# Kernel optimization log

Measured on AMD Instinct MI355X. Metric: run time of the kernel, lower is better.

## Reference

```python
import jax, jax.numpy as jnp
import numpy as np

D_MODEL = 768
D_INNER = 1536      # d_model * expand
D_STATE = 128
D_CONV = 4
HEADDIM = 64
NHEADS = 24         # d_inner / headdim
CONV_DIM = D_INNER + 2 * D_STATE          # 1792
D_IN_PROJ = 2 * D_INNER + 2 * D_STATE + NHEADS  # 3352
EPS = 1e-5
BATCH, SEQLEN = 4, 2048


def setup_inputs() -> dict:
    key = jax.random.key(0)
    ks = jax.random.split(key, 8)
    u = jax.random.normal(ks[0], (BATCH, SEQLEN, D_MODEL), dtype=jnp.float32)
    W_in = jax.random.normal(ks[1], (D_IN_PROJ, D_MODEL), dtype=jnp.float32) * 0.02
    conv_w = jax.random.normal(ks[2], (CONV_DIM, D_CONV), dtype=jnp.float32) * 0.2
    conv_b = jnp.zeros((CONV_DIM,), dtype=jnp.float32)
    # dt_bias = inverse-softplus of dt sampled log-uniformly in [dt_min, dt_max]
    dt = jnp.exp(jax.random.uniform(ks[3], (NHEADS,)) * (np.log(0.1) - np.log(0.001)) + np.log(0.001))
    dt = jnp.clip(dt, 1e-4, None)
    dt_bias = dt + jnp.log(-jnp.expm1(-dt))
    A_log = jnp.log(jax.random.uniform(ks[4], (NHEADS,), minval=1.0, maxval=16.0))
    D = jnp.ones((NHEADS,), dtype=jnp.float32)
    norm_w = jnp.ones((D_INNER,), dtype=jnp.float32)
    W_out = jax.random.normal(ks[5], (D_MODEL, D_INNER), dtype=jnp.float32) * 0.02
    return {"u": u, "W_in": W_in, "conv_w": conv_w, "conv_b": conv_b,
            "dt_bias": dt_bias, "A_log": A_log, "D": D, "norm_w": norm_w, "W_out": W_out}


def reference(u, W_in, conv_w, conv_b, dt_bias, A_log, D, norm_w, W_out):
    b, L, _ = u.shape
    zxbcdt = jnp.einsum('bld,ed->ble', u, W_in)  # (b, L, 3352)
    z = zxbcdt[..., :D_INNER]
    xBC = zxbcdt[..., D_INNER:D_INNER + CONV_DIM]
    dt = zxbcdt[..., D_INNER + CONV_DIM:]        # (b, L, nheads)

    # causal depthwise conv1d (kernel width 4), then SiLU
    xp = jnp.pad(xBC, ((0, 0), (D_CONV - 1, 0), (0, 0)))
    xBC = sum(xp[:, k:k + L, :] * conv_w[:, k] for k in range(D_CONV)) + conv_b
    xBC = jax.nn.silu(xBC)

    x = xBC[..., :D_INNER].reshape(b, L, NHEADS, HEADDIM)
    B = xBC[..., D_INNER:D_INNER + D_STATE]      # (b, L, n)  (ngroups=1)
    C = xBC[..., D_INNER + D_STATE:]             # (b, L, n)

    dt = jax.nn.softplus(dt + dt_bias)           # (b, L, h)
    A = -jnp.exp(A_log)                          # (h,)
    dA = jnp.exp(dt * A)                         # (b, L, h)

    def step(h, inp):
        dA_t, dt_t, x_t, B_t, C_t = inp
        # h: (b, h, p, n)
        h = h * dA_t[:, :, None, None] + jnp.einsum('bhp,bh,bn->bhpn', x_t, dt_t, B_t)
        y = jnp.einsum('bhpn,bn->bhp', h, C_t)
        return h, y

    xs = (jnp.swapaxes(dA, 0, 1), jnp.swapaxes(dt, 0, 1), jnp.swapaxes(x, 0, 1),
          jnp.swapaxes(B, 0, 1), jnp.swapaxes(C, 0, 1))
    h0 = jnp.zeros((b, NHEADS, HEADDIM, D_STATE), dtype=u.dtype)
    _, ys = jax.lax.scan(step, h0, xs)           # ys: (L, b, h, p)
    y = jnp.swapaxes(ys, 0, 1)                   # (b, L, h, p)

    y = y + D[None, None, :, None] * x           # skip connection
    y = y.reshape(b, L, D_INNER)

    # RMSNorm then gate with silu(z)
    y = norm_w * y * jax.lax.rsqrt(jnp.mean(y * y, axis=-1, keepdims=True) + EPS)
    y = y * jax.nn.silu(z)
    return jnp.einsum('bld,ed->ble', y, W_out)
```

## Files before the change

kernel.cpp:

```cpp
#include <hip/hip_runtime.h>
#include <hip/hip_bf16.h>

typedef __bf16 bf16x8 __attribute__((ext_vector_type(8)));
typedef float f32x4 __attribute__((ext_vector_type(4)));
typedef unsigned int u32x4 __attribute__((ext_vector_type(4)));

#define MTOT    8192
#define DMODEL  768
#define DINNER  1536
#define DSTATE  128
#define NHEADS  24
#define CONVDIM 1792
#define LDZ     3328
#define SEQ     2048
#define CHUNK   128
#define NCHUNK  16
#define NBH     96

#define NU   (MTOT*DMODEL)
#define NWI  (LDZ*DMODEL)
#define NWO  (DMODEL*DINNER)
#define NWD  (32*DMODEL)

__device__ __forceinline__ void gl2lds16(const __hip_bfloat16* g, __hip_bfloat16* l) {
  __builtin_amdgcn_global_load_lds((const __attribute__((address_space(1))) void*)g,
                                   (__attribute__((address_space(3))) void*)l, 16, 0, 0);
}

__global__ __launch_bounds__(256) void cvt_bf16(const float* __restrict__ u, const float* __restrict__ Wi,
                                                const float* __restrict__ Wo,
                                                __hip_bfloat16* __restrict__ ub, __hip_bfloat16* __restrict__ wib,
                                                __hip_bfloat16* __restrict__ wob,
                                                __hip_bfloat16* __restrict__ wdh, __hip_bfloat16* __restrict__ wdl) {
  int i = blockIdx.x * 256 + threadIdx.x;
  if (i < NU) ub[i] = __float2bfloat16(u[i]);
  else if (i < NU + NWI) { int k = i - NU; wib[k] = __float2bfloat16(Wi[k]); }
  else if (i < NU + NWI + NWO) { int k = i - NU - NWI; wob[k] = __float2bfloat16(Wo[k]); }
  else if (i < NU + NWI + NWO + 2 * NWD) {
    int k = i - NU - NWI - NWO;
    int lo = (k >= NWD);
    if (lo) k -= NWD;
    int row = k / DMODEL, col = k - row * DMODEL;
    float w = (row < NHEADS) ? Wi[(size_t)(LDZ + row) * DMODEL + col] : 0.f;
    __hip_bfloat16 h = __float2bfloat16(w);
    if (!lo) wdh[k] = h;
    else wdl[k] = __float2bfloat16(w - __bfloat162float(h));
  }
}

__global__ __launch_bounds__(256, 2) void gemm_bt(const __hip_bfloat16* __restrict__ A,
                                                  const __hip_bfloat16* __restrict__ B,
                                                  float* __restrict__ C, int lda, int ldb, int ldc, int nk) {
  __shared__ __align__(16) __hip_bfloat16 As[2][128 * 32];
  __shared__ __align__(16) __hip_bfloat16 Bs[2][128 * 32];
  const int tid = threadIdx.x;
  const int lane = tid & 63, wid = tid >> 6;
  const int wm = wid >> 1, wn = wid & 1;
  const int bm = blockIdx.y, bn = blockIdx.x;
  const int sr = lane >> 2;
  const int sc = (((lane & 3) ^ ((sr >> 1) & 3))) * 8;
  const int row0 = wid * 32 + sr;
  const __hip_bfloat16* Ag0 = A + (size_t)(bm * 128 + row0) * lda + sc;
  const __hip_bfloat16* Ag1 = Ag0 + (size_t)16 * lda;
  const __hip_bfloat16* Bg0 = B + (size_t)(bn * 128 + row0) * ldb + sc;
  const __hip_bfloat16* Bg1 = Bg0 + (size_t)16 * ldb;
  f32x4 acc[4][4] = {};
  const int lr = lane & 15, lk = lane >> 4;
  const int arow = wm * 64 + lr, brow = wn * 64 + lr;
  const int ach = (lk ^ ((lr >> 1) & 3)) * 8;
#define STAGE(buf, ks)                                   \
  do {                                                   \
    gl2lds16(Ag0 + (ks) * 32, &As[buf][(wid * 32) * 32]);      \
    gl2lds16(Ag1 + (ks) * 32, &As[buf][(wid * 32 + 16) * 32]); \
    gl2lds16(Bg0 + (ks) * 32, &Bs[buf][(wid * 32) * 32]);      \
    gl2lds16(Bg1 + (ks) * 32, &Bs[buf][(wid * 32 + 16) * 32]); \
  } while (0)
  STAGE(0, 0);
  __syncthreads();
  for (int ks = 0; ks < nk; ++ks) {
    const int cur = ks & 1;
    if (ks + 1 < nk) STAGE(cur ^ 1, ks + 1);
    bf16x8 af[4], bfr[4];
#pragma unroll
    for (int i = 0; i < 4; ++i) {
      af[i] = *(const bf16x8*)&As[cur][(arow + i * 16) * 32 + ach];
      bfr[i] = *(const bf16x8*)&Bs[cur][(brow + i * 16) * 32 + ach];
    }
#pragma unroll
    for (int i = 0; i < 4; ++i)
#pragma unroll
      for (int j = 0; j < 4; ++j)
        acc[i][j] = __builtin_amdgcn_mfma_f32_16x16x32_bf16(af[i], bfr[j], acc[i][j], 0, 0, 0);
    __syncthreads();
  }
#undef STAGE
  const int crow0 = bm * 128 + wm * 64 + lk * 4;
  const int ccol0 = bn * 128 + wn * 64 + lr;
#pragma unroll
  for (int i = 0; i < 4; ++i)
#pragma unroll
    for (int j = 0; j < 4; ++j)
#pragma unroll
      for (int r = 0; r < 4; ++r)
        C[(size_t)(crow0 + i * 16 + r) * ldc + ccol0 + j * 16] = acc[i][j][r];
}

__global__ __launch_bounds__(256) void dt_mfma(const float* __restrict__ u,
                                               const __hip_bfloat16* __restrict__ wdh,
                                               const __hip_bfloat16* __restrict__ wdl,
                                               const float* __restrict__ dtb, const float* __restrict__ alog,
                                               float* __restrict__ dtS, float* __restrict__ dtA) {
  __shared__ __align__(16) __hip_bfloat16 Uh[64 * 32];
  __shared__ __align__(16) __hip_bfloat16 Ul[64 * 32];
  const int tid = threadIdx.x;
  const int lane = tid & 63, wid = tid >> 6;
  const int lr = lane & 15, lk = lane >> 4;
  const int bm = blockIdx.x;
  const int r = tid >> 2, c0 = (tid & 3) * 8;
  const float* usrc = u + (size_t)(bm * 64 + r) * DMODEL + c0;
  f32x4 acc[2] = {};
  for (int ks = 0; ks < DMODEL / 32; ++ks) {
    float4 v0 = *(const float4*)(usrc + ks * 32);
    float4 v1 = *(const float4*)(usrc + ks * 32 + 4);
    bf16x8 hi, lo;
    const float* vf = (const float*)&v0;
#pragma unroll
    for (int e = 0; e < 4; ++e) {
      __hip_bfloat16 h = __float2bfloat16(vf[e]);
      hi[e] = *(__bf16*)&h;
      __hip_bfloat16 l2 = __float2bfloat16(vf[e] - __bfloat162float(h));
      lo[e] = *(__bf16*)&l2;
    }
    vf = (const float*)&v1;
#pragma unroll
    for (int e = 0; e < 4; ++e) {
      __hip_bfloat16 h = __float2bfloat16(vf[e]);
      hi[4 + e] = *(__bf16*)&h;
      __hip_bfloat16 l2 = __float2bfloat16(vf[e] - __bfloat162float(h));
      lo[4 + e] = *(__bf16*)&l2;
    }
    *(bf16x8*)&Uh[r * 32 + c0] = hi;
    *(bf16x8*)&Ul[r * 32 + c0] = lo;
    __syncthreads();
    bf16x8 ah = *(const bf16x8*)&Uh[(wid * 16 + lr) * 32 + lk * 8];
    bf16x8 al = *(const bf16x8*)&Ul[(wid * 16 + lr) * 32 + lk * 8];
#pragma unroll
    for (int j = 0; j < 2; ++j) {
      bf16x8 bh = *(const bf16x8*)(wdh + (size_t)(j * 16 + lr) * DMODEL + ks * 32 + lk * 8);
      bf16x8 bl = *(const bf16x8*)(wdl + (size_t)(j * 16 + lr) * DMODEL + ks * 32 + lk * 8);
      acc[j] = __builtin_amdgcn_mfma_f32_16x16x32_bf16(ah, bh, acc[j], 0, 0, 0);
      acc[j] = __builtin_amdgcn_mfma_f32_16x16x32_bf16(ah, bl, acc[j], 0, 0, 0);
      acc[j] = __builtin_amdgcn_mfma_f32_16x16x32_bf16(al, bh, acc[j], 0, 0, 0);
    }
    __syncthreads();
  }
#pragma unroll
  for (int j = 0; j < 2; ++j) {
    int col = j * 16 + lr;
    if (col < NHEADS) {
      float nA = -expf(alog[col]);
      float bia = dtb[col];
#pragma unroll
      for (int rr = 0; rr < 4; ++rr) {
        int row = bm * 64 + wid * 16 + lk * 4 + rr;
        float x = acc[j][rr] + bia;
        float dt = (x > 20.f) ? x : log1pf(expf(x));
        dtS[(size_t)row * NHEADS + col] = dt;
        dtA[(size_t)row * NHEADS + col] = nA * dt;
      }
    }
  }
}

__global__ __launch_bounds__(256) void cumsum_kernel(const float* __restrict__ dtA, float* __restrict__ scum,
                                                     float* __restrict__ cdec) {
  int bc = blockIdx.x;
  int b = bc >> 4, c = bc & 15;
  __shared__ float buf[CHUNK * NHEADS];
  int m0 = b * SEQ + c * CHUNK;
  for (int t = threadIdx.x; t < CHUNK * NHEADS; t += 256)
    buf[t] = dtA[(size_t)m0 * NHEADS + t];
  __syncthreads();
  if (threadIdx.x < NHEADS) {
    int h = threadIdx.x;
    float run = 0.f;
    float* dst = scum + ((size_t)bc * NHEADS + h) * CHUNK;
    for (int j = 0; j < CHUNK; ++j) { run += buf[j * NHEADS + h]; dst[j] = run; }
    cdec[(b * NHEADS + h) * NCHUNK + c] = __expf(run);
  }
}

__global__ __launch_bounds__(256) void conv_fused(const float* __restrict__ zxb, const float* __restrict__ cw,
                                                  const float* __restrict__ cb, const float* __restrict__ dtS,
                                                  __hip_bfloat16* __restrict__ Xd, __hip_bfloat16* __restrict__ Bb,
                                                  __hip_bfloat16* __restrict__ Cb, __hip_bfloat16* __restrict__ XdT,
                                                  __hip_bfloat16* __restrict__ Bt) {
  __shared__ __hip_bfloat16 t[64][72];
  __shared__ float dts_sh[64];
  const int c0 = blockIdx.x * 64, m0 = blockIdx.y * 64;
  const int b = m0 >> 11, l0 = m0 & (SEQ - 1);
  const int tid = threadIdx.x;
  const int c = tid & 63, rg = tid >> 6;
  const int gc = c0 + c;
  const bool isX = (c0 < DINNER);
  if (isX && tid < 64) dts_sh[tid] = dtS[(size_t)(m0 + tid) * NHEADS + (c0 >> 6)];
  const float4 w = *(const float4*)(cw + (size_t)gc * 4);
  const float bias = cb[gc];
  const float* src = zxb + (size_t)(m0 + rg * 16) * LDZ + DINNER + gc;
  const int lbase = l0 + rg * 16;
  float v0 = (lbase >= 3) ? src[-3 * (ptrdiff_t)LDZ] : 0.f;
  float v1 = (lbase >= 2) ? src[-2 * (ptrdiff_t)LDZ] : 0.f;
  float v2 = (lbase >= 1) ? src[-1 * (ptrdiff_t)LDZ] : 0.f;
  __syncthreads();
#pragma unroll
  for (int r = 0; r < 16; ++r) {
    float v3 = src[(ptrdiff_t)r * LDZ];
    float a = bias + v0 * w.x + v1 * w.y + v2 * w.z + v3 * w.w;
    float sv = a / (1.f + __expf(-a));
    int lm = rg * 16 + r;
    __hip_bfloat16 val = __float2bfloat16(isX ? dts_sh[lm] * sv : sv);
    t[lm][c] = val;
    int m = m0 + lm;
    if (isX) Xd[(size_t)m * DINNER + gc] = val;
    else if (gc < DINNER + DSTATE) Bb[(size_t)m * DSTATE + gc - DINNER] = val;
    else Cb[(size_t)m * DSTATE + gc - DINNER - DSTATE] = val;
    v0 = v1; v1 = v2; v2 = v3;
  }
  __syncthreads();
  if (c0 < DINNER + DSTATE) {
    int r2 = tid >> 2, cc = (tid & 3) * 16;
    __hip_bfloat16 tmp[16] __attribute__((aligned(16)));
#pragma unroll
    for (int k = 0; k < 16; ++k) tmp[k] = t[cc + k][r2];
    __hip_bfloat16* dst = isX ? XdT + ((size_t)(b * DINNER + c0 + r2)) * SEQ + l0 + cc
                              : Bt + ((size_t)(b * DSTATE + (c0 - DINNER) + r2)) * SEQ + l0 + cc;
    *(u32x4*)dst = *(u32x4*)&tmp[0];
    *(u32x4*)(dst + 8) = *(u32x4*)&tmp[8];
  }
}

__global__ __launch_bounds__(256, 2) void state_gemm(const __hip_bfloat16* __restrict__ XdT,
                                                     const __hip_bfloat16* __restrict__ Bt,
                                                     const float* __restrict__ scum,
                                                     __hip_bfloat16* __restrict__ cstat) {
  __shared__ __align__(16) __hip_bfloat16 Xw[64 * 136];
  __shared__ __align__(16) __hip_bfloat16 Bts[128 * 136];
  __shared__ float rS[CHUNK];
  int bid = blockIdx.x;
  int c = bid & 15, bh = bid >> 4;
  int b = bh / NHEADS, h = bh % NHEADS;
  const float* sp = scum + ((size_t)(b * NCHUNK + c) * NHEADS + h) * CHUNK;
  int tid = threadIdx.x;
  if (tid < CHUNK) rS[tid] = __expf(sp[CHUNK - 1] - sp[tid]);
  {
    int n = tid >> 1, jc = (tid & 1) * 64;
    const __hip_bfloat16* g = Bt + ((size_t)(b * DSTATE + n)) * SEQ + c * CHUNK + jc;
#pragma unroll
    for (int q = 0; q < 8; ++q) *(u32x4*)&Bts[n * 136 + jc + q * 8] = *(const u32x4*)(g + q * 8);
  }
  __syncthreads();
  {
    int p = tid >> 2, jc = (tid & 3) * 32;
    const __hip_bfloat16* g = XdT + ((size_t)((b * NHEADS + h) * 64 + p)) * SEQ + c * CHUNK + jc;
#pragma unroll
    for (int q = 0; q < 4; ++q) {
      bf16x8 vv = *(const bf16x8*)(g + q * 8);
      bf16x8 ov;
#pragma unroll
      for (int e = 0; e < 8; ++e) ov[e] = (__bf16)((float)vv[e] * rS[jc + q * 8 + e]);
      *(bf16x8*)&Xw[p * 136 + jc + q * 8] = ov;
    }
  }
  __syncthreads();
  const int lane = tid & 63, wid = tid >> 6;
  const int wm = wid >> 1, wn = wid & 1;
  const int lr = lane & 15, lk = lane >> 4;
  f32x4 acc[2][4] = {};
#pragma unroll
  for (int ks = 0; ks < 4; ++ks) {
    bf16x8 af[2], bq[4];
#pragma unroll
    for (int i = 0; i < 2; ++i) af[i] = *(const bf16x8*)&Xw[(wm * 32 + i * 16 + lr) * 136 + ks * 32 + lk * 8];
#pragma unroll
    for (int j = 0; j < 4; ++j) bq[j] = *(const bf16x8*)&Bts[(wn * 64 + j * 16 + lr) * 136 + ks * 32 + lk * 8];
#pragma unroll
    for (int i = 0; i < 2; ++i)
#pragma unroll
      for (int j = 0; j < 4; ++j)
        acc[i][j] = __builtin_amdgcn_mfma_f32_16x16x32_bf16(af[i], bq[j], acc[i][j], 0, 0, 0);
  }
  __hip_bfloat16* dst = cstat + (size_t)bid * 8192;
#pragma unroll
  for (int i = 0; i < 2; ++i)
#pragma unroll
    for (int j = 0; j < 4; ++j)
#pragma unroll
      for (int r = 0; r < 4; ++r)
        dst[(wm * 32 + i * 16 + lk * 4 + r) * 128 + wn * 64 + j * 16 + lr] = __float2bfloat16(acc[i][j][r]);
}

__global__ __launch_bounds__(256) void scanB(__hip_bfloat16* __restrict__ cstat, const float* __restrict__ cdec) {
  const int bh = blockIdx.x >> 3, sl = blockIdx.x & 7;
  const int base = sl * 1024 + threadIdx.x * 4;
  float hreg[4] = {0.f, 0.f, 0.f, 0.f};
  for (int c = 0; c < NCHUNK; ++c) {
    __hip_bfloat16* p = cstat + (size_t)(bh * NCHUNK + c) * 8192 + base;
    const float P = cdec[bh * NCHUNK + c];
    __hip_bfloat16 tmp[4], hs[4];
    *(uint2*)tmp = *(const uint2*)p;
#pragma unroll
    for (int j = 0; j < 4; ++j) hs[j] = __float2bfloat16(hreg[j]);
    *(uint2*)p = *(uint2*)hs;
#pragma unroll
    for (int j = 0; j < 4; ++j) hreg[j] = fmaf(hreg[j], P, __bfloat162float(tmp[j]));
  }
}

template <int JE>
__global__ __launch_bounds__(256, 2) void ssd_y(const __hip_bfloat16* __restrict__ Cb,
                                                const __hip_bfloat16* __restrict__ Bb,
                                                const __hip_bfloat16* __restrict__ XdT,
                                                const __hip_bfloat16* __restrict__ Xd,
                                                const __hip_bfloat16* __restrict__ cstat,
                                                const float* __restrict__ scum,
                                                const float* __restrict__ dtS, const float* __restrict__ Dvec,
                                                float* __restrict__ zxb) {
  constexpr int HI = JE - 64;
  constexpr int JW = JE / 2;
  constexpr int FJ = JW / 16;
  constexpr int KJ = JE / 32;
  __shared__ __align__(16) __hip_bfloat16 Cs[64 * 136];
  __shared__ __align__(16) __hip_bfloat16 Bs[JE * 136];
  __shared__ __align__(16) __hip_bfloat16 R3[64 * 136];
  __shared__ float sS[CHUNK];
  int bid = blockIdx.x;
  int c = bid & 15, bh = bid >> 4;
  int b = bh / NHEADS, h = bh % NHEADS;
  int m0 = b * SEQ + c * CHUNK;
  int tid = threadIdx.x;
  const float* sp = scum + ((size_t)(b * NCHUNK + c) * NHEADS + h) * CHUNK;
  if (tid < CHUNK) sS[tid] = sp[tid];
  {
    int r = tid >> 2, nc = (tid & 3) * 32;
    const __hip_bfloat16* g = Cb + (size_t)(m0 + HI + r) * DSTATE + nc;
#pragma unroll
    for (int q = 0; q < 4; ++q) *(u32x4*)&Cs[r * 136 + nc + q * 8] = *(const u32x4*)(g + q * 8);
  }
  if (JE == 64) {
    int r = tid >> 2, nc = (tid & 3) * 32;
    const __hip_bfloat16* g = Bb + (size_t)(m0 + r) * DSTATE + nc;
#pragma unroll
    for (int q = 0; q < 4; ++q) *(u32x4*)&Bs[r * 136 + nc + q * 8] = *(const u32x4*)(g + q * 8);
  } else {
    int r = tid >> 1, nc = (tid & 1) * 64;
    const __hip_bfloat16* g = Bb + (size_t)(m0 + r) * DSTATE + nc;
#pragma unroll
    for (int q = 0; q < 8; ++q) *(u32x4*)&Bs[r * 136 + nc + q * 8] = *(const u32x4*)(g + q * 8);
  }
  {
    int p = tid >> 2, nc = (tid & 3) * 32;
    const __hip_bfloat16* g = cstat + (size_t)bid * 8192 + p * 128 + nc;
#pragma unroll
    for (int q = 0; q < 4; ++q) *(u32x4*)&R3[p * 136 + nc + q * 8] = *(const u32x4*)(g + q * 8);
  }
  __syncthreads();
  const int lane = tid & 63, wid = tid >> 6;
  const int wm = wid >> 1, wn = wid & 1;
  const int lr = lane & 15, lk = lane >> 4;
  f32x4 Gacc[2][FJ] = {};
  f32x4 Uacc[2][2] = {};
#pragma unroll
  for (int ks = 0; ks < 4; ++ks) {
    bf16x8 af[2], bq[2];
#pragma unroll
    for (int i = 0; i < 2; ++i) af[i] = *(const bf16x8*)&Cs[(wm * 32 + i * 16 + lr) * 136 + ks * 32 + lk * 8];
#pragma unroll
    for (int j = 0; j < 2; ++j) bq[j] = *(const bf16x8*)&R3[(wn * 32 + j * 16 + lr) * 136 + ks * 32 + lk * 8];
#pragma unroll
    for (int i = 0; i < 2; ++i)
#pragma unroll
      for (int j = 0; j < 2; ++j)
        Uacc[i][j] = __builtin_amdgcn_mfma_f32_16x16x32_bf16(af[i], bq[j], Uacc[i][j], 0, 0, 0);
  }
#pragma unroll
  for (int ks = 0; ks < 4; ++ks) {
    bf16x8 af[2], bq[FJ];
#pragma unroll
    for (int i = 0; i < 2; ++i) af[i] = *(const bf16x8*)&Cs[(wm * 32 + i * 16 + lr) * 136 + ks * 32 + lk * 8];
#pragma unroll
    for (int j = 0; j < FJ; ++j) bq[j] = *(const bf16x8*)&Bs[(wn * JW + j * 16 + lr) * 136 + ks * 32 + lk * 8];
#pragma unroll
    for (int i = 0; i < 2; ++i)
#pragma unroll
      for (int j = 0; j < FJ; ++j)
        Gacc[i][j] = __builtin_amdgcn_mfma_f32_16x16x32_bf16(af[i], bq[j], Gacc[i][j], 0, 0, 0);
  }
  __syncthreads();
  {
    float siv[2][4];
#pragma unroll
    for (int i = 0; i < 2; ++i)
#pragma unroll
      for (int r = 0; r < 4; ++r) siv[i][r] = sS[HI + wm * 32 + i * 16 + lk * 4 + r];
#pragma unroll
    for (int i = 0; i < 2; ++i)
#pragma unroll
      for (int j = 0; j < FJ; ++j) {
        int gj = wn * JW + j * 16 + lr;
        float sj = sS[gj];
#pragma unroll
        for (int r = 0; r < 4; ++r) {
          int il = wm * 32 + i * 16 + lk * 4 + r;
          int gi = HI + il;
          float mv = (gj <= gi) ? Gacc[i][j][r] * __expf(siv[i][r] - sj) : 0.f;
          Cs[il * 136 + gj] = __float2bfloat16(mv);
        }
      }
  }
  {
    int p = tid >> 2, jc = (tid & 3) * (JE / 4);
    const __hip_bfloat16* g = XdT + ((size_t)((b * NHEADS + h) * 64 + p)) * SEQ + c * CHUNK + jc;
#pragma unroll
    for (int q = 0; q < JE / 32; ++q) *(u32x4*)&R3[p * 136 + jc + q * 8] = *(const u32x4*)(g + q * 8);
  }
  __syncthreads();
  f32x4 Yacc[2][2] = {};
#pragma unroll
  for (int ks = 0; ks < KJ; ++ks) {
    bf16x8 af[2], bq[2];
#pragma unroll
    for (int i = 0; i < 2; ++i) af[i] = *(const bf16x8*)&Cs[(wm * 32 + i * 16 + lr) * 136 + ks * 32 + lk * 8];
#pragma unroll
    for (int j = 0; j < 2; ++j) bq[j] = *(const bf16x8*)&R3[(wn * 32 + j * 16 + lr) * 136 + ks * 32 + lk * 8];
#pragma unroll
    for (int i = 0; i < 2; ++i)
#pragma unroll
      for (int j = 0; j < 2; ++j)
        Yacc[i][j] = __builtin_amdgcn_mfma_f32_16x16x32_bf16(af[i], bq[j], Yacc[i][j], 0, 0, 0);
  }
  const float Dh = Dvec[h];
#pragma unroll
  for (int i = 0; i < 2; ++i)
#pragma unroll
    for (int r = 0; r < 4; ++r) {
      int il = wm * 32 + i * 16 + lk * 4 + r;
      int gi = HI + il;
      int m = m0 + gi;
      float ei = __expf(sS[gi]);
      float dt = dtS[(size_t)m * NHEADS + h];
#pragma unroll
      for (int j = 0; j < 2; ++j) {
        int p = wn * 32 + j * 16 + lr;
        float xv = (float)Xd[(size_t)m * DINNER + h * 64 + p] / dt;
        zxb[(size_t)m * LDZ + DINNER + h * 64 + p] = Yacc[i][j][r] + ei * Uacc[i][j][r] + Dh * xv;
      }
    }
}

__global__ __launch_bounds__(256) void norm_gate(const float* __restrict__ zxb, const float* __restrict__ nw,
                                                 __hip_bfloat16* __restrict__ yg) {
  const int m = blockIdx.x, tid = threadIdx.x;
  const float* zr = zxb + (size_t)m * LDZ;
  const float* yr = zr + DINNER;
  float yv[6], zv[6];
  float ss = 0.f;
#pragma unroll
  for (int jj = 0; jj < 6; ++jj) {
    int i = tid + jj * 256;
    yv[jj] = yr[i];
    zv[jj] = zr[i];
    ss = fmaf(yv[jj], yv[jj], ss);
  }
#pragma unroll
  for (int o = 32; o > 0; o >>= 1) ss += __shfl_down(ss, o);
  __shared__ float red[4];
  if ((tid & 63) == 0) red[tid >> 6] = ss;
  __syncthreads();
  float tot = red[0] + red[1] + red[2] + red[3];
  float r = rsqrtf(tot * (1.f / 1536.f) + 1e-5f);
#pragma unroll
  for (int jj = 0; jj < 6; ++jj) {
    int i = tid + jj * 256;
    float z = zv[jj];
    float g = z / (1.f + __expf(-z));
    yg[(size_t)m * DINNER + i] = __float2bfloat16(nw[i] * yv[jj] * r * g);
  }
}

extern "C" void kernel_launch(void* const* d_in, const int* in_sizes, int n_in,
                              void* d_out, int out_size, void* d_ws, size_t ws_size,
                              hipStream_t stream) {
  (void)in_sizes; (void)n_in; (void)out_size; (void)ws_size;
  const float* u       = (const float*)d_in[0];
  const float* W_in    = (const float*)d_in[1];
  const float* conv_w  = (const float*)d_in[2];
  const float* conv_b  = (const float*)d_in[3];
  const float* dt_bias = (const float*)d_in[4];
  const float* A_log   = (const float*)d_in[5];
  const float* Dvec    = (const float*)d_in[6];
  const float* norm_w  = (const float*)d_in[7];
  const float* W_out   = (const float*)d_in[8];
  float* out = (float*)d_out;

  float* zxb = (float*)d_ws;
  __hip_bfloat16* cstatb = (__hip_bfloat16*)(zxb + (size_t)MTOT * LDZ);
  float* dtS  = (float*)(cstatb + (size_t)NBH * NCHUNK * 8192);
  float* dtA  = dtS + (size_t)MTOT * NHEADS;
  float* scum = dtA + (size_t)MTOT * NHEADS;
  float* cdec = scum + (size_t)MTOT * NHEADS;
  __hip_bfloat16* ub  = (__hip_bfloat16*)(cdec + NBH * NCHUNK);
  __hip_bfloat16* wib = ub + (size_t)NU;
  __hip_bfloat16* wob = wib + (size_t)NWI;
  __hip_bfloat16* wdh = wob + (size_t)NWO;
  __hip_bfloat16* wdl = wdh + (size_t)NWD;
  __hip_bfloat16* Xd  = wdl + (size_t)NWD;
  __hip_bfloat16* Bb  = Xd + (size_t)MTOT * DINNER;
  __hip_bfloat16* Cb  = Bb + (size_t)MTOT * DSTATE;
  __hip_bfloat16* XdT = Cb + (size_t)MTOT * DSTATE;
  __hip_bfloat16* Bt  = XdT + (size_t)MTOT * DINNER;
  __hip_bfloat16* yg  = Xd;

  cvt_bf16<<<(NU + NWI + NWO + 2 * NWD + 255) / 256, 256, 0, stream>>>(u, W_in, W_out, ub, wib, wob, wdh, wdl);
  gemm_bt<<<dim3(LDZ / 128, MTOT / 128), 256, 0, stream>>>(ub, wib, zxb, DMODEL, DMODEL, LDZ, DMODEL / 32);
  dt_mfma<<<MTOT / 64, 256, 0, stream>>>(u, wdh, wdl, dt_bias, A_log, dtS, dtA);
  cumsum_kernel<<<64, 256, 0, stream>>>(dtA, scum, cdec);
  conv_fused<<<dim3(CONVDIM / 64, MTOT / 64), 256, 0, stream>>>(zxb, conv_w, conv_b, dtS, Xd, Bb, Cb, XdT, Bt);
  state_gemm<<<NBH * NCHUNK, 256, 0, stream>>>(XdT, Bt, scum, cstatb);
  scanB<<<NBH * 8, 256, 0, stream>>>(cstatb, cdec);
  ssd_y<64><<<NBH * NCHUNK, 256, 0, stream>>>(Cb, Bb, XdT, Xd, cstatb, scum, dtS, Dvec, zxb);
  ssd_y<128><<<NBH * NCHUNK, 256, 0, stream>>>(Cb, Bb, XdT, Xd, cstatb, scum, dtS, Dvec, zxb);
  norm_gate<<<MTOT, 256, 0, stream>>>(zxb, norm_w, yg);
  gemm_bt<<<dim3(DMODEL / 128, MTOT / 128), 256, 0, stream>>>(yg, wob, out, DINNER, DINNER, DMODEL, DINNER / 32);
}
```

Measured before the change: 350.1 us.

## Add 256x256 tiled in-proj GEMM with bf16 intermediate buffer and vectorized norm

Replaces the 128x128 input-projection GEMM with a new 512-thread 256x256-tile kernel. It uses a 64-wide K step, grouped block swizzling, priority hints around the MFMA phases and split prefetch stages. The zxb intermediate (z, xBC and y) is now stored in bf16 instead of fp32, which halves its traffic in conv, ssd_y and norm_gate. norm_gate is rewritten to use 192 threads with 8-wide vector loads and stores. The trade-off is lower precision in the intermediates, and the 3328-column output only gives 13 column tiles, so a 416-block grid at one block per CU may leave occupancy low.

```diff
diff --git a/kernel.cpp b/kernel.cpp
--- a/kernel.cpp
+++ b/kernel.cpp
@@ -46,6 +46,119 @@
     if (!lo) wdh[k] = h;
     else wdl[k] = __float2bfloat16(w - __bfloat162float(h));
   }
+}
+
+#define BAR256()                          \
+  __builtin_amdgcn_sched_barrier(0);      \
+  __builtin_amdgcn_s_barrier();           \
+  __builtin_amdgcn_sched_barrier(0)
+
+template <typename OutT>
+__global__ __launch_bounds__(512, 1) void gemm256(const __hip_bfloat16* __restrict__ A,
+                                                  const __hip_bfloat16* __restrict__ B,
+                                                  OutT* __restrict__ C, int lda, int ldb, int ldc,
+                                                  int nkt, int nbn) {
+  __shared__ __align__(16) __hip_bfloat16 As[2][256 * 64];
+  __shared__ __align__(16) __hip_bfloat16 Bs[2][256 * 64];
+  const int tid = threadIdx.x;
+  const int lane = tid & 63, wid = tid >> 6;
+  const int wm = wid >> 2, wn = wid & 3;
+  const int lr = lane & 15, lk = lane >> 4;
+  const int cpx = (int)gridDim.x >> 3;
+  const int swz = ((int)blockIdx.x & 7) * cpx + ((int)blockIdx.x >> 3);
+  const int bn = swz % nbn, bm = swz / nbn;
+  const int srow = tid >> 3;
+  const int scol = ((tid & 7) ^ (srow & 7)) * 8;
+  const __hip_bfloat16* Ag = A + (size_t)(bm * 256 + srow) * lda + scol;
+  const __hip_bfloat16* Bg = B + (size_t)(bn * 256 + srow) * ldb + scol;
+  const int ldst = wid * 512;
+  const int rpc = lr & 7;
+
+#define STG256(bf, kt, i)                                                             \
+  do {                                                                                \
+    gl2lds16(Ag + (size_t)(i) * 64 * lda + (size_t)(kt) * 64, &As[bf][(i) * 4096 + ldst]); \
+    gl2lds16(Bg + (size_t)(i) * 64 * ldb + (size_t)(kt) * 64, &Bs[bf][(i) * 4096 + ldst]); \
+  } while (0)
+#define LDA256(bf, mf, ks) (*(const bf16x8*)&As[bf][(wm * 128 + (mf) * 16 + lr) * 64 + (((ks) * 4 + lk) ^ rpc) * 8])
+#define LDB256(bf, nf, ks) (*(const bf16x8*)&Bs[bf][(wn * 64 + (nf) * 16 + lr) * 64 + (((ks) * 4 + lk) ^ rpc) * 8])
+
+  f32x4 acc[8][4] = {};
+  bf16x8 aF[8], bF0[4], bF1[4];
+
+  STG256(0, 0, 0); STG256(0, 0, 1); STG256(0, 0, 2); STG256(0, 0, 3);
+  asm volatile("s_waitcnt vmcnt(0)" ::: "memory");
+  BAR256();
+
+  for (int kt = 0; kt < nkt; ++kt) {
+    const int c = kt & 1;
+    const bool pf = (kt + 1 < nkt);
+#pragma unroll
+    for (int i = 0; i < 4; ++i) { aF[i * 2] = LDA256(c, i, 0); aF[i * 2 + 1] = LDA256(c, i, 1); }
+#pragma unroll
+    for (int j = 0; j < 2; ++j) { bF0[j * 2] = LDB256(c, j, 0); bF0[j * 2 + 1] = LDB256(c, j, 1); }
+    if (pf) { STG256(c ^ 1, kt + 1, 0); STG256(c ^ 1, kt + 1, 1); }
+    BAR256();
+    __builtin_amdgcn_s_setprio(1);
+#pragma unroll
+    for (int i = 0; i < 4; ++i)
+#pragma unroll
+      for (int j = 0; j < 2; ++j) {
+        acc[i][j] = __builtin_amdgcn_mfma_f32_16x16x32_bf16(aF[i * 2], bF0[j * 2], acc[i][j], 0, 0, 0);
+        acc[i][j] = __builtin_amdgcn_mfma_f32_16x16x32_bf16(aF[i * 2 + 1], bF0[j * 2 + 1], acc[i][j], 0, 0, 0);
+      }
+    __builtin_amdgcn_s_setprio(0);
+    BAR256();
+#pragma unroll
+    for (int j = 0; j < 2; ++j) { bF1[j * 2] = LDB256(c, 2 + j, 0); bF1[j * 2 + 1] = LDB256(c, 2 + j, 1); }
+    if (pf) { STG256(c ^ 1, kt + 1, 2); STG256(c ^ 1, kt + 1, 3); }
+    BAR256();
+    __builtin_amdgcn_s_setprio(1);
+#pragma unroll
+    for (int i = 0; i < 4; ++i)
+#pragma unroll
+      for (int j = 0; j < 2; ++j) {
+        acc[i][2 + j] = __builtin_amdgcn_mfma_f32_16x16x32_bf16(aF[i * 2], bF1[j * 2], acc[i][2 + j], 0, 0, 0);
+        acc[i][2 + j] = __builtin_amdgcn_mfma_f32_16x16x32_bf16(aF[i * 2 + 1], bF1[j * 2 + 1], acc[i][2 + j], 0, 0, 0);
+      }
+    __builtin_amdgcn_s_setprio(0);
+    BAR256();
+#pragma unroll
+    for (int i = 0; i < 4; ++i) { aF[i * 2] = LDA256(c, 4 + i, 0); aF[i * 2 + 1] = LDA256(c, 4 + i, 1); }
+    BAR256();
+    __builtin_amdgcn_s_setprio(1);
+#pragma unroll
+    for (int i = 0; i < 4; ++i)
+#pragma unroll
+      for (int j = 0; j < 2; ++j) {
+        acc[4 + i][2 + j] = __builtin_amdgcn_mfma_f32_16x16x32_bf16(aF[i * 2], bF1[j * 2], acc[4 + i][2 + j], 0, 0, 0);
+        acc[4 + i][2 + j] = __builtin_amdgcn_mfma_f32_16x16x32_bf16(aF[i * 2 + 1], bF1[j * 2 + 1], acc[4 + i][2 + j], 0, 0, 0);
+      }
+    __builtin_amdgcn_s_setprio(0);
+    BAR256();
+    __builtin_amdgcn_s_setprio(1);
+#pragma unroll
+    for (int i = 0; i < 4; ++i)
+#pragma unroll
+      for (int j = 0; j < 2; ++j) {
+        acc[4 + i][j] = __builtin_amdgcn_mfma_f32_16x16x32_bf16(aF[i * 2], bF0[j * 2], acc[4 + i][j], 0, 0, 0);
+        acc[4 + i][j] = __builtin_amdgcn_mfma_f32_16x16x32_bf16(aF[i * 2 + 1], bF0[j * 2 + 1], acc[4 + i][j], 0, 0, 0);
+      }
+    __builtin_amdgcn_s_setprio(0);
+    if (pf) { asm volatile("s_waitcnt vmcnt(0)" ::: "memory"); }
+    BAR256();
+  }
+#undef STG256
+#undef LDA256
+#undef LDB256
+  const int crow0 = bm * 256 + wm * 128 + lk * 4;
+  const int ccol0 = bn * 256 + wn * 64 + lr;
+#pragma unroll
+  for (int mf = 0; mf < 8; ++mf)
+#pragma unroll
+    for (int nf = 0; nf < 4; ++nf)
+#pragma unroll
+      for (int r = 0; r < 4; ++r)
+        C[(size_t)(crow0 + mf * 16 + r) * ldc + ccol0 + nf * 16] = (OutT)acc[mf][nf][r];
 }
 
 __global__ __launch_bounds__(256, 2) void gemm_bt(const __hip_bfloat16* __restrict__ A,
@@ -68,8 +181,8 @@
   const int lr = lane & 15, lk = lane >> 4;
   const int arow = wm * 64 + lr, brow = wn * 64 + lr;
   const int ach = (lk ^ ((lr >> 1) & 3)) * 8;
-#define STAGE(buf, ks)                                   \
-  do {                                                   \
+#define STAGE(buf, ks)                                         \
+  do {                                                         \
     gl2lds16(Ag0 + (ks) * 32, &As[buf][(wid * 32) * 32]);      \
     gl2lds16(Ag1 + (ks) * 32, &As[buf][(wid * 32 + 16) * 32]); \
     gl2lds16(Bg0 + (ks) * 32, &Bs[buf][(wid * 32) * 32]);      \
@@ -190,7 +303,8 @@
   }
 }
 
-__global__ __launch_bounds__(256) void conv_fused(const float* __restrict__ zxb, const float* __restrict__ cw,
+__global__ __launch_bounds__(256) void conv_fused(const __hip_bfloat16* __restrict__ zxb,
+                                                  const float* __restrict__ cw,
                                                   const float* __restrict__ cb, const float* __restrict__ dtS,
                                                   __hip_bfloat16* __restrict__ Xd, __hip_bfloat16* __restrict__ Bb,
                                                   __hip_bfloat16* __restrict__ Cb, __hip_bfloat16* __restrict__ XdT,
@@ -206,15 +320,15 @@
   if (isX && tid < 64) dts_sh[tid] = dtS[(size_t)(m0 + tid) * NHEADS + (c0 >> 6)];
   const float4 w = *(const float4*)(cw + (size_t)gc * 4);
   const float bias = cb[gc];
-  const float* src = zxb + (size_t)(m0 + rg * 16) * LDZ + DINNER + gc;
+  const __hip_bfloat16* src = zxb + (size_t)(m0 + rg * 16) * LDZ + DINNER + gc;
   const int lbase = l0 + rg * 16;
-  float v0 = (lbase >= 3) ? src[-3 * (ptrdiff_t)LDZ] : 0.f;
-  float v1 = (lbase >= 2) ? src[-2 * (ptrdiff_t)LDZ] : 0.f;
-  float v2 = (lbase >= 1) ? src[-1 * (ptrdiff_t)LDZ] : 0.f;
+  float v0 = (lbase >= 3) ? __bfloat162float(src[-3 * (ptrdiff_t)LDZ]) : 0.f;
+  float v1 = (lbase >= 2) ? __bfloat162float(src[-2 * (ptrdiff_t)LDZ]) : 0.f;
+  float v2 = (lbase >= 1) ? __bfloat162float(src[-1 * (ptrdiff_t)LDZ]) : 0.f;
   __syncthreads();
 #pragma unroll
   for (int r = 0; r < 16; ++r) {
-    float v3 = src[(ptrdiff_t)r * LDZ];
+    float v3 = __bfloat162float(src[(ptrdiff_t)r * LDZ]);
     float a = bias + v0 * w.x + v1 * w.y + v2 * w.z + v3 * w.w;
     float sv = a / (1.f + __expf(-a));
     int lm = rg * 16 + r;
@@ -324,7 +438,7 @@
                                                 const __hip_bfloat16* __restrict__ cstat,
                                                 const float* __restrict__ scum,
                                                 const float* __restrict__ dtS, const float* __restrict__ Dvec,
-                                                float* __restrict__ zxb) {
+                                                __hip_bfloat16* __restrict__ zxb) {
   constexpr int HI = JE - 64;
   constexpr int JW = JE / 2;
   constexpr int FJ = JW / 16;
@@ -452,39 +566,46 @@
       for (int j = 0; j < 2; ++j) {
         int p = wn * 32 + j * 16 + lr;
         float xv = (float)Xd[(size_t)m * DINNER + h * 64 + p] / dt;
-        zxb[(size_t)m * LDZ + DINNER + h * 64 + p] = Yacc[i][j][r] + ei * Uacc[i][j][r] + Dh * xv;
+        zxb[(size_t)m * LDZ + DINNER + h * 64 + p] =
+            __float2bfloat16(Yacc[i][j][r] + ei * Uacc[i][j][r] + Dh * xv);
       }
     }
 }
 
-__global__ __launch_bounds__(256) void norm_gate(const float* __restrict__ zxb, const float* __restrict__ nw,
+__global__ __launch_bounds__(192) void norm_gate(const __hip_bfloat16* __restrict__ zxb,
+                                                 const float* __restrict__ nw,
                                                  __hip_bfloat16* __restrict__ yg) {
   const int m = blockIdx.x, tid = threadIdx.x;
-  const float* zr = zxb + (size_t)m * LDZ;
-  const float* yr = zr + DINNER;
-  float yv[6], zv[6];
+  const __hip_bfloat16* zr = zxb + (size_t)m * LDZ;
+  const __hip_bfloat16* yr = zr + DINNER;
+  bf16x8 y8 = *(const bf16x8*)&yr[tid * 8];
+  bf16x8 z8 = *(const bf16x8*)&zr[tid * 8];
+  float yv[8], zv[8];
   float ss = 0.f;
 #pragma unroll
-  for (int jj = 0; jj < 6; ++jj) {
-    int i = tid + jj * 256;
-    yv[jj] = yr[i];
-    zv[jj] = zr[i];
-    ss = fmaf(yv[jj], yv[jj], ss);
+  for (int e = 0; e < 8; ++e) {
+    yv[e] = (float)y8[e];
+    zv[e] = (float)z8[e];
+    ss = fmaf(yv[e], yv[e], ss);
   }
 #pragma unroll
   for (int o = 32; o > 0; o >>= 1) ss += __shfl_down(ss, o);
-  __shared__ float red[4];
+  __shared__ float red[3];
   if ((tid & 63) == 0) red[tid >> 6] = ss;
   __syncthreads();
-  float tot = red[0] + red[1] + red[2] + red[3];
+  float tot = red[0] + red[1] + red[2];
   float r = rsqrtf(tot * (1.f / 1536.f) + 1e-5f);
-#pragma unroll
-  for (int jj = 0; jj < 6; ++jj) {
-    int i = tid + jj * 256;
-    float z = zv[jj];
-    float g = z / (1.f + __expf(-z));
-    yg[(size_t)m * DINNER + i] = __float2bfloat16(nw[i] * yv[jj] * r * g);
-  }
+  float4 w0 = *(const float4*)&nw[tid * 8];
+  float4 w1 = *(const float4*)&nw[tid * 8 + 4];
+  const float* wf = (const float*)&w0;
+  bf16x8 o8;
+#pragma unroll
+  for (int e = 0; e < 8; ++e) {
+    float wv = (e < 4) ? wf[e] : ((const float*)&w1)[e - 4];
+    float g = zv[e] / (1.f + __expf(-zv[e]));
+    o8[e] = (__bf16)(wv * yv[e] * r * g);
+  }
+  *(bf16x8*)&yg[(size_t)m * DINNER + tid * 8] = o8;
 }
 
 extern "C" void kernel_launch(void* const* d_in, const int* in_sizes, int n_in,
@@ -502,8 +623,8 @@
   const float* W_out   = (const float*)d_in[8];
   float* out = (float*)d_out;
 
-  float* zxb = (float*)d_ws;
-  __hip_bfloat16* cstatb = (__hip_bfloat16*)(zxb + (size_t)MTOT * LDZ);
+  __hip_bfloat16* zxbb = (__hip_bfloat16*)d_ws;
+  __hip_bfloat16* cstatb = zxbb + (size_t)MTOT * LDZ;
   float* dtS  = (float*)(cstatb + (size_t)NBH * NCHUNK * 8192);
   float* dtA  = dtS + (size_t)MTOT * NHEADS;
   float* scum = dtA + (size_t)MTOT * NHEADS;
@@ -521,14 +642,15 @@
   __hip_bfloat16* yg  = Xd;
 
   cvt_bf16<<<(NU + NWI + NWO + 2 * NWD + 255) / 256, 256, 0, stream>>>(u, W_in, W_out, ub, wib, wob, wdh, wdl);
-  gemm_bt<<<dim3(LDZ / 128, MTOT / 128), 256, 0, stream>>>(ub, wib, zxb, DMODEL, DMODEL, LDZ, DMODEL / 32);
+  gemm256<__hip_bfloat16><<<(LDZ / 256) * (MTOT / 256), 512, 0, stream>>>(ub, wib, zxbb, DMODEL, DMODEL, LDZ,
+                                                                          DMODEL / 64, LDZ / 256);
   dt_mfma<<<MTOT / 64, 256, 0, stream>>>(u, wdh, wdl, dt_bias, A_log, dtS, dtA);
   cumsum_kernel<<<64, 256, 0, stream>>>(dtA, scum, cdec);
-  conv_fused<<<dim3(CONVDIM / 64, MTOT / 64), 256, 0, stream>>>(zxb, conv_w, conv_b, dtS, Xd, Bb, Cb, XdT, Bt);
+  conv_fused<<<dim3(CONVDIM / 64, MTOT / 64), 256, 0, stream>>>(zxbb, conv_w, conv_b, dtS, Xd, Bb, Cb, XdT, Bt);
   state_gemm<<<NBH * NCHUNK, 256, 0, stream>>>(XdT, Bt, scum, cstatb);
   scanB<<<NBH * 8, 256, 0, stream>>>(cstatb, cdec);
-  ssd_y<64><<<NBH * NCHUNK, 256, 0, stream>>>(Cb, Bb, XdT, Xd, cstatb, scum, dtS, Dvec, zxb);
-  ssd_y<128><<<NBH * NCHUNK, 256, 0, stream>>>(Cb, Bb, XdT, Xd, cstatb, scum, dtS, Dvec, zxb);
-  norm_gate<<<MTOT, 256, 0, stream>>>(zxb, norm_w, yg);
+  ssd_y<64><<<NBH * NCHUNK, 256, 0, stream>>>(Cb, Bb, XdT, Xd, cstatb, scum, dtS, Dvec, zxbb);
+  ssd_y<128><<<NBH * NCHUNK, 256, 0, stream>>>(Cb, Bb, XdT, Xd, cstatb, scum, dtS, Dvec, zxbb);
+  norm_gate<<<MTOT, 192, 0, stream>>>(zxbb, norm_w, yg);
   gemm_bt<<<dim3(DMODEL / 128, MTOT / 128), 256, 0, stream>>>(yg, wob, out, DINNER, DINNER, DMODEL, DINNER / 32);
 }
```

After: 338.2 us. 3.4% less time.

## Replace GEMMs with 4-stage ring-buffered templated kernel and store zxb in bf16

Applied to the files above, without the earlier changes.

Replaces the double-buffered 128x128 GEMM with a templated kernel that keeps a 4-slot LDS ring, uses explicit vmcnt waits, raises MFMA priority with setprio, and applies an XCD-aware block swizzle. The input projection now uses 256x256 tiles with 512 threads. The intermediate zxb buffer changes from fp32 to bf16, which halves the bytes moved by the projection GEMM, conv, ssd_y and norm_gate. norm_gate is vectorised to 8 bf16 elements per thread with 192 threads. The cost is lower precision in z, xBC and y, plus larger LDS use, since the 4-stage 256x256 tiles take 128 KB.

```diff
diff --git a/kernel.cpp b/kernel.cpp
--- a/kernel.cpp
+++ b/kernel.cpp
@@ -48,61 +48,83 @@
   }
 }
 
-__global__ __launch_bounds__(256, 2) void gemm_bt(const __hip_bfloat16* __restrict__ A,
-                                                  const __hip_bfloat16* __restrict__ B,
-                                                  float* __restrict__ C, int lda, int ldb, int ldc, int nk) {
-  __shared__ __align__(16) __hip_bfloat16 As[2][128 * 32];
-  __shared__ __align__(16) __hip_bfloat16 Bs[2][128 * 32];
+#define STG_R(s)                                                                               \
+  {                                                                                            \
+    const int sl_ = (s) & 3;                                                                   \
+    _Pragma("unroll") for (int i_ = 0; i_ < CA; ++i_)                                          \
+        gl2lds16(Ag + (size_t)(i_ * RA) * lda + (s) * 32, &As[sl_][i_ * (T * 8) + tid * 8]);   \
+    _Pragma("unroll") for (int i_ = 0; i_ < CB; ++i_)                                          \
+        gl2lds16(Bg + (size_t)(i_ * RA) * ldb + (s) * 32, &Bs[sl_][i_ * (T * 8) + tid * 8]);   \
+  }
+
+#define PHASE_R(t, DOSTG, VMW)                                                                 \
+  {                                                                                            \
+    if (DOSTG) STG_R((t) + 3);                                                                 \
+    const int sl_ = (t) & 3;                                                                   \
+    bf16x8 fa_[FM], fb_[FN];                                                                   \
+    _Pragma("unroll") for (int i_ = 0; i_ < FM; ++i_)                                          \
+        fa_[i_] = *(const bf16x8*)&As[sl_][(wm * PM + i_ * 16 + lr) * 32 + rch];               \
+    _Pragma("unroll") for (int j_ = 0; j_ < FN; ++j_)                                          \
+        fb_[j_] = *(const bf16x8*)&Bs[sl_][(wn * PN + j_ * 16 + lr) * 32 + rch];               \
+    __builtin_amdgcn_s_setprio(1);                                                             \
+    _Pragma("unroll") for (int i_ = 0; i_ < FM; ++i_)                                          \
+        _Pragma("unroll") for (int j_ = 0; j_ < FN; ++j_)                                      \
+            acc[i_][j_] =                                                                      \
+                __builtin_amdgcn_mfma_f32_16x16x32_bf16(fa_[i_], fb_[j_], acc[i_][j_], 0, 0, 0); \
+    __builtin_amdgcn_s_setprio(0);                                                             \
+    VMW;                                                                                       \
+    __builtin_amdgcn_sched_barrier(0);                                                         \
+    __builtin_amdgcn_s_barrier();                                                              \
+    __builtin_amdgcn_sched_barrier(0);                                                         \
+  }
+
+template <int BM, int BN, int WGM, int WGN, typename OutT>
+__global__ __launch_bounds__(WGM * WGN * 64, 2) void gemm_ring(const __hip_bfloat16* __restrict__ A,
+                                                               const __hip_bfloat16* __restrict__ B,
+                                                               OutT* __restrict__ C, int lda, int ldb,
+                                                               int ldc, int nsub, int nbn) {
+  constexpr int T = WGM * WGN * 64;
+  constexpr int PM = BM / WGM, PN = BN / WGN;
+  constexpr int FM = PM / 16, FN = PN / 16;
+  constexpr int CA = (BM * 64) / (T * 16);
+  constexpr int CB = (BN * 64) / (T * 16);
+  constexpr int RA = T / 4;
+  __shared__ __align__(16) __hip_bfloat16 As[4][BM * 32];
+  __shared__ __align__(16) __hip_bfloat16 Bs[4][BN * 32];
   const int tid = threadIdx.x;
   const int lane = tid & 63, wid = tid >> 6;
-  const int wm = wid >> 1, wn = wid & 1;
-  const int bm = blockIdx.y, bn = blockIdx.x;
-  const int sr = lane >> 2;
-  const int sc = (((lane & 3) ^ ((sr >> 1) & 3))) * 8;
-  const int row0 = wid * 32 + sr;
-  const __hip_bfloat16* Ag0 = A + (size_t)(bm * 128 + row0) * lda + sc;
-  const __hip_bfloat16* Ag1 = Ag0 + (size_t)16 * lda;
-  const __hip_bfloat16* Bg0 = B + (size_t)(bn * 128 + row0) * ldb + sc;
-  const __hip_bfloat16* Bg1 = Bg0 + (size_t)16 * ldb;
-  f32x4 acc[4][4] = {};
+  const int wm = wid / WGN, wn = wid % WGN;
   const int lr = lane & 15, lk = lane >> 4;
-  const int arow = wm * 64 + lr, brow = wn * 64 + lr;
-  const int ach = (lk ^ ((lr >> 1) & 3)) * 8;
-#define STAGE(buf, ks)                                   \
-  do {                                                   \
-    gl2lds16(Ag0 + (ks) * 32, &As[buf][(wid * 32) * 32]);      \
-    gl2lds16(Ag1 + (ks) * 32, &As[buf][(wid * 32 + 16) * 32]); \
-    gl2lds16(Bg0 + (ks) * 32, &Bs[buf][(wid * 32) * 32]);      \
-    gl2lds16(Bg1 + (ks) * 32, &Bs[buf][(wid * 32 + 16) * 32]); \
-  } while (0)
-  STAGE(0, 0);
-  __syncthreads();
-  for (int ks = 0; ks < nk; ++ks) {
-    const int cur = ks & 1;
-    if (ks + 1 < nk) STAGE(cur ^ 1, ks + 1);
-    bf16x8 af[4], bfr[4];
-#pragma unroll
-    for (int i = 0; i < 4; ++i) {
-      af[i] = *(const bf16x8*)&As[cur][(arow + i * 16) * 32 + ach];
-      bfr[i] = *(const bf16x8*)&Bs[cur][(brow + i * 16) * 32 + ach];
-    }
-#pragma unroll
-    for (int i = 0; i < 4; ++i)
-#pragma unroll
-      for (int j = 0; j < 4; ++j)
-        acc[i][j] = __builtin_amdgcn_mfma_f32_16x16x32_bf16(af[i], bfr[j], acc[i][j], 0, 0, 0);
-    __syncthreads();
-  }
-#undef STAGE
-  const int crow0 = bm * 128 + wm * 64 + lk * 4;
-  const int ccol0 = bn * 128 + wn * 64 + lr;
-#pragma unroll
-  for (int i = 0; i < 4; ++i)
-#pragma unroll
-    for (int j = 0; j < 4; ++j)
+  const int cpx = (int)gridDim.x >> 3;
+  const int swz = ((int)blockIdx.x & 7) * cpx + ((int)blockIdx.x >> 3);
+  const int bn = swz % nbn, bm = swz / nbn;
+  const int srow = tid >> 2;
+  const int scol = ((tid & 3) ^ ((tid >> 3) & 3)) * 8;
+  const __hip_bfloat16* Ag = A + (size_t)(bm * BM + srow) * lda + scol;
+  const __hip_bfloat16* Bg = B + (size_t)(bn * BN + srow) * ldb + scol;
+  const int rch = (lk ^ ((lr >> 1) & 3)) * 8;
+  f32x4 acc[FM][FN] = {};
+
+  STG_R(0); STG_R(1); STG_R(2);
+  asm volatile("s_waitcnt vmcnt(8)" ::: "memory");
+  __builtin_amdgcn_sched_barrier(0);
+  __builtin_amdgcn_s_barrier();
+  __builtin_amdgcn_sched_barrier(0);
+  int t = 0;
+  for (; t < nsub - 3; ++t) PHASE_R(t, true, asm volatile("s_waitcnt vmcnt(8)" ::: "memory"));
+  PHASE_R(t, false, asm volatile("s_waitcnt vmcnt(4)" ::: "memory")); ++t;
+  PHASE_R(t, false, asm volatile("s_waitcnt vmcnt(0)" ::: "memory")); ++t;
+  PHASE_R(t, false, (void)0);
+
+  const int crow0 = bm * BM + wm * PM + lk * 4;
+  const int ccol0 = bn * BN + wn * PN + lr;
+#pragma unroll
+  for (int mf = 0; mf < FM; ++mf)
+#pragma unroll
+    for (int nf = 0; nf < FN; ++nf)
 #pragma unroll
       for (int r = 0; r < 4; ++r)
-        C[(size_t)(crow0 + i * 16 + r) * ldc + ccol0 + j * 16] = acc[i][j][r];
+        C[(size_t)(crow0 + mf * 16 + r) * ldc + ccol0 + nf * 16] = (OutT)acc[mf][nf][r];
 }
 
 __global__ __launch_bounds__(256) void dt_mfma(const float* __restrict__ u,
@@ -190,7 +212,8 @@
   }
 }
 
-__global__ __launch_bounds__(256) void conv_fused(const float* __restrict__ zxb, const float* __restrict__ cw,
+__global__ __launch_bounds__(256) void conv_fused(const __hip_bfloat16* __restrict__ zxb,
+                                                  const float* __restrict__ cw,
                                                   const float* __restrict__ cb, const float* __restrict__ dtS,
                                                   __hip_bfloat16* __restrict__ Xd, __hip_bfloat16* __restrict__ Bb,
                                                   __hip_bfloat16* __restrict__ Cb, __hip_bfloat16* __restrict__ XdT,
@@ -206,15 +229,15 @@
   if (isX && tid < 64) dts_sh[tid] = dtS[(size_t)(m0 + tid) * NHEADS + (c0 >> 6)];
   const float4 w = *(const float4*)(cw + (size_t)gc * 4);
   const float bias = cb[gc];
-  const float* src = zxb + (size_t)(m0 + rg * 16) * LDZ + DINNER + gc;
+  const __hip_bfloat16* src = zxb + (size_t)(m0 + rg * 16) * LDZ + DINNER + gc;
   const int lbase = l0 + rg * 16;
-  float v0 = (lbase >= 3) ? src[-3 * (ptrdiff_t)LDZ] : 0.f;
-  float v1 = (lbase >= 2) ? src[-2 * (ptrdiff_t)LDZ] : 0.f;
-  float v2 = (lbase >= 1) ? src[-1 * (ptrdiff_t)LDZ] : 0.f;
+  float v0 = (lbase >= 3) ? __bfloat162float(src[-3 * (ptrdiff_t)LDZ]) : 0.f;
+  float v1 = (lbase >= 2) ? __bfloat162float(src[-2 * (ptrdiff_t)LDZ]) : 0.f;
+  float v2 = (lbase >= 1) ? __bfloat162float(src[-1 * (ptrdiff_t)LDZ]) : 0.f;
   __syncthreads();
 #pragma unroll
   for (int r = 0; r < 16; ++r) {
-    float v3 = src[(ptrdiff_t)r * LDZ];
+    float v3 = __bfloat162float(src[(ptrdiff_t)r * LDZ]);
     float a = bias + v0 * w.x + v1 * w.y + v2 * w.z + v3 * w.w;
     float sv = a / (1.f + __expf(-a));
     int lm = rg * 16 + r;
@@ -324,7 +347,7 @@
                                                 const __hip_bfloat16* __restrict__ cstat,
                                                 const float* __restrict__ scum,
                                                 const float* __restrict__ dtS, const float* __restrict__ Dvec,
-                                                float* __restrict__ zxb) {
+                                                __hip_bfloat16* __restrict__ zxb) {
   constexpr int HI = JE - 64;
   constexpr int JW = JE / 2;
   constexpr int FJ = JW / 16;
@@ -452,39 +475,46 @@
       for (int j = 0; j < 2; ++j) {
         int p = wn * 32 + j * 16 + lr;
         float xv = (float)Xd[(size_t)m * DINNER + h * 64 + p] / dt;
-        zxb[(size_t)m * LDZ + DINNER + h * 64 + p] = Yacc[i][j][r] + ei * Uacc[i][j][r] + Dh * xv;
+        zxb[(size_t)m * LDZ + DINNER + h * 64 + p] =
+            __float2bfloat16(Yacc[i][j][r] + ei * Uacc[i][j][r] + Dh * xv);
       }
     }
 }
 
-__global__ __launch_bounds__(256) void norm_gate(const float* __restrict__ zxb, const float* __restrict__ nw,
+__global__ __launch_bounds__(192) void norm_gate(const __hip_bfloat16* __restrict__ zxb,
+                                                 const float* __restrict__ nw,
                                                  __hip_bfloat16* __restrict__ yg) {
   const int m = blockIdx.x, tid = threadIdx.x;
-  const float* zr = zxb + (size_t)m * LDZ;
-  const float* yr = zr + DINNER;
-  float yv[6], zv[6];
+  const __hip_bfloat16* zr = zxb + (size_t)m * LDZ;
+  const __hip_bfloat16* yr = zr + DINNER;
+  bf16x8 y8 = *(const bf16x8*)&yr[tid * 8];
+  bf16x8 z8 = *(const bf16x8*)&zr[tid * 8];
+  float yv[8], zv[8];
   float ss = 0.f;
 #pragma unroll
-  for (int jj = 0; jj < 6; ++jj) {
-    int i = tid + jj * 256;
-    yv[jj] = yr[i];
-    zv[jj] = zr[i];
-    ss = fmaf(yv[jj], yv[jj], ss);
+  for (int e = 0; e < 8; ++e) {
+    yv[e] = (float)y8[e];
+    zv[e] = (float)z8[e];
+    ss = fmaf(yv[e], yv[e], ss);
   }
 #pragma unroll
   for (int o = 32; o > 0; o >>= 1) ss += __shfl_down(ss, o);
-  __shared__ float red[4];
+  __shared__ float red[3];
   if ((tid & 63) == 0) red[tid >> 6] = ss;
   __syncthreads();
-  float tot = red[0] + red[1] + red[2] + red[3];
+  float tot = red[0] + red[1] + red[2];
   float r = rsqrtf(tot * (1.f / 1536.f) + 1e-5f);
-#pragma unroll
-  for (int jj = 0; jj < 6; ++jj) {
-    int i = tid + jj * 256;
-    float z = zv[jj];
-    float g = z / (1.f + __expf(-z));
-    yg[(size_t)m * DINNER + i] = __float2bfloat16(nw[i] * yv[jj] * r * g);
-  }
+  float4 w0 = *(const float4*)&nw[tid * 8];
+  float4 w1 = *(const float4*)&nw[tid * 8 + 4];
+  const float* wf = (const float*)&w0;
+  bf16x8 o8;
+#pragma unroll
+  for (int e = 0; e < 8; ++e) {
+    float wv = (e < 4) ? wf[e] : ((const float*)&w1)[e - 4];
+    float g = zv[e] / (1.f + __expf(-zv[e]));
+    o8[e] = (__bf16)(wv * yv[e] * r * g);
+  }
+  *(bf16x8*)&yg[(size_t)m * DINNER + tid * 8] = o8;
 }
 
 extern "C" void kernel_launch(void* const* d_in, const int* in_sizes, int n_in,
@@ -502,8 +532,8 @@
   const float* W_out   = (const float*)d_in[8];
   float* out = (float*)d_out;
 
-  float* zxb = (float*)d_ws;
-  __hip_bfloat16* cstatb = (__hip_bfloat16*)(zxb + (size_t)MTOT * LDZ);
+  __hip_bfloat16* zxbb = (__hip_bfloat16*)d_ws;
+  __hip_bfloat16* cstatb = zxbb + (size_t)MTOT * LDZ;
   float* dtS  = (float*)(cstatb + (size_t)NBH * NCHUNK * 8192);
   float* dtA  = dtS + (size_t)MTOT * NHEADS;
   float* scum = dtA + (size_t)MTOT * NHEADS;
@@ -521,14 +551,16 @@
   __hip_bfloat16* yg  = Xd;
 
   cvt_bf16<<<(NU + NWI + NWO + 2 * NWD + 255) / 256, 256, 0, stream>>>(u, W_in, W_out, ub, wib, wob, wdh, wdl);
-  gemm_bt<<<dim3(LDZ / 128, MTOT / 128), 256, 0, stream>>>(ub, wib, zxb, DMODEL, DMODEL, LDZ, DMODEL / 32);
+  gemm_ring<256, 256, 2, 4, __hip_bfloat16><<<(LDZ / 256) * (MTOT / 256), 512, 0, stream>>>(
+      ub, wib, zxbb, DMODEL, DMODEL, LDZ, DMODEL / 32, LDZ / 256);
   dt_mfma<<<MTOT / 64, 256, 0, stream>>>(u, wdh, wdl, dt_bias, A_log, dtS, dtA);
   cumsum_kernel<<<64, 256, 0, stream>>>(dtA, scum, cdec);
-  conv_fused<<<dim3(CONVDIM / 64, MTOT / 64), 256, 0, stream>>>(zxb, conv_w, conv_b, dtS, Xd, Bb, Cb, XdT, Bt);
+  conv_fused<<<dim3(CONVDIM / 64, MTOT / 64), 256, 0, stream>>>(zxbb, conv_w, conv_b, dtS, Xd, Bb, Cb, XdT, Bt);
   state_gemm<<<NBH * NCHUNK, 256, 0, stream>>>(XdT, Bt, scum, cstatb);
   scanB<<<NBH * 8, 256, 0, stream>>>(cstatb, cdec);
-  ssd_y<64><<<NBH * NCHUNK, 256, 0, stream>>>(Cb, Bb, XdT, Xd, cstatb, scum, dtS, Dvec, zxb);
-  ssd_y<128><<<NBH * NCHUNK, 256, 0, stream>>>(Cb, Bb, XdT, Xd, cstatb, scum, dtS, Dvec, zxb);
-  norm_gate<<<MTOT, 256, 0, stream>>>(zxb, norm_w, yg);
-  gemm_bt<<<dim3(DMODEL / 128, MTOT / 128), 256, 0, stream>>>(yg, wob, out, DINNER, DINNER, DMODEL, DINNER / 32);
-}
+  ssd_y<64><<<NBH * NCHUNK, 256, 0, stream>>>(Cb, Bb, XdT, Xd, cstatb, scum, dtS, Dvec, zxbb);
+  ssd_y<128><<<NBH * NCHUNK, 256, 0, stream>>>(Cb, Bb, XdT, Xd, cstatb, scum, dtS, Dvec, zxbb);
+  norm_gate<<<MTOT, 192, 0, stream>>>(zxbb, norm_w, yg);
+  gemm_ring<128, 128, 2, 2, float><<<(DMODEL / 128) * (MTOT / 128), 256, 0, stream>>>(
+      yg, wob, out, DINNER, DINNER, DMODEL, DINNER / 32, DMODEL / 128);
+}
```

Measured after the change: 339.1 us. 3.2% less time.
